# Optimization experiments

Hardware: AMD Instinct MI355X
Metric: run time of the kernel (lower is better)

Reference implementation:

```python
import jax, jax.numpy as jnp
import numpy as np

N_QUBITS = 8
INPUT_DIM = 256
SEQ_LEN = 256
BATCH = 512


def qgate(theta, x):
    # Closed-form expectation of the PennyLane circuit:
    #   RX(x_i) then RY(theta_i) on each wire (from |0>), then CNOT chain 0->1->...->n-1,
    #   measure <Z_k>.  Single-wire <Z_j> = cos(x_j) * cos(theta_j); CNOT chain maps
    #   Z_k -> Z_0 Z_1 ... Z_k in the Heisenberg picture, so on the product state
    #   <Z_k> = prod_{j<=k} cos(x_j) cos(theta_j).
    # x: (B, n_wires), theta: (n_wires,)
    return jnp.cumprod(jnp.cos(x) * jnp.cos(theta), axis=-1)


def setup_inputs() -> dict:
    key = jax.random.key(0)
    ks = jax.random.split(key, 14)
    d_in = INPUT_DIM + N_QUBITS  # concat([x, hx]) -> 264
    lin_scale = 1.0 / np.sqrt(d_in)
    inp = {
        "inputs": jax.random.normal(ks[0], (SEQ_LEN, BATCH, INPUT_DIM), dtype=jnp.float32),
        "Wf": jax.random.normal(ks[1], (N_QUBITS, d_in), dtype=jnp.float32) * lin_scale,
        "bf": jax.random.normal(ks[2], (N_QUBITS,), dtype=jnp.float32) * lin_scale,
        "Wi": jax.random.normal(ks[3], (N_QUBITS, d_in), dtype=jnp.float32) * lin_scale,
        "bi": jax.random.normal(ks[4], (N_QUBITS,), dtype=jnp.float32) * lin_scale,
        "Wu": jax.random.normal(ks[5], (N_QUBITS, d_in), dtype=jnp.float32) * lin_scale,
        "bu": jax.random.normal(ks[6], (N_QUBITS,), dtype=jnp.float32) * lin_scale,
        "Wo": jax.random.normal(ks[7], (N_QUBITS, d_in), dtype=jnp.float32) * lin_scale,
        "bo": jax.random.normal(ks[8], (N_QUBITS,), dtype=jnp.float32) * lin_scale,
        "pf": jax.random.normal(ks[9], (N_QUBITS,), dtype=jnp.float32),
        "pi_": jax.random.normal(ks[10], (N_QUBITS,), dtype=jnp.float32),
        "pu": jax.random.normal(ks[11], (N_QUBITS,), dtype=jnp.float32),
        "po": jax.random.normal(ks[12], (N_QUBITS,), dtype=jnp.float32),
    }
    return inp


def reference(inputs, Wf, bf, Wi, bi, Wu, bu, Wo, bo, pf, pi_, pu, po):
    B = inputs.shape[1]
    H = pf.shape[0]  # hidden_dim == n_qubits

    def step(carry, x):
        hx, cx = carry
        comb = jnp.concatenate([x, hx], axis=1)  # (B, input_dim + H)
        f = jax.nn.sigmoid(qgate(pf, comb @ Wf.T + bf))
        i = jax.nn.sigmoid(qgate(pi_, comb @ Wi.T + bi))
        g = jnp.tanh(qgate(pu, comb @ Wu.T + bu))
        o = jax.nn.sigmoid(qgate(po, comb @ Wo.T + bo))
        cx = f * cx + i * g
        hx = o * jnp.tanh(cx)
        return (hx, cx), hx

    init = (jnp.zeros((B, H), dtype=inputs.dtype), jnp.zeros((B, H), dtype=inputs.dtype))
    (hx, cx), stacked = jax.lax.scan(step, init, inputs)
    return stacked, hx, cx
```

## Files before the change

kernel.cpp:

```cpp
#include <hip/hip_runtime.h>
#include <hip/hip_bf16.h>


#define SEQ   256
#define BATCH 512
#define DIN   256
#define NROWS (SEQ * BATCH)
#define DCOMB 264
#define MCHUNKS 4

typedef __attribute__((ext_vector_type(8))) short short8;
typedef __attribute__((ext_vector_type(4))) float f32x4;
typedef __attribute__((ext_vector_type(2))) float f32x2;

__device__ __forceinline__ short f2bf(float f) {
    union { __hip_bfloat16 h; short s; } u;
    u.h = __float2bfloat16(f);
    return u.s;
}
__device__ __forceinline__ float bf2f(short s) {
    union { short s; __hip_bfloat16 h; } u;
    u.s = s;
    return __bfloat162float(u.h);
}

__device__ __forceinline__ short8 pack8(float4 a, float4 b) {
    union { short8 s8; int i[4]; } u;
    union { __hip_bfloat162 h; int i; } v;
    v.h = __float22bfloat162_rn(make_float2(a.x, a.y)); u.i[0] = v.i;
    v.h = __float22bfloat162_rn(make_float2(a.z, a.w)); u.i[1] = v.i;
    v.h = __float22bfloat162_rn(make_float2(b.x, b.y)); u.i[2] = v.i;
    v.h = __float22bfloat162_rn(make_float2(b.z, b.w)); u.i[3] = v.i;
    return u.s8;
}

__global__ __launch_bounds__(256) void qlstm_gemm(
    const float* __restrict__ X,
    const float* __restrict__ Wf, const float* __restrict__ Wi,
    const float* __restrict__ Wu, const float* __restrict__ Wo,
    const float* __restrict__ bfv, const float* __restrict__ biv,
    const float* __restrict__ buv, const float* __restrict__ bov,
    float* __restrict__ Z)
{
    const int l   = threadIdx.x & 63;
    const int wid = threadIdx.x >> 6;
    const int lm  = l & 15;
    const int lk  = l >> 4;

    const float* Wg[4] = {Wf, Wi, Wu, Wo};
    const float* Bg[4] = {bfv, biv, buv, bov};

    short8 Bhi[2][8], Blo[2][8];
    float bias[2];
    #pragma unroll
    for (int nt = 0; nt < 2; ++nt) {
        const int c = nt * 16 + lm;
        const float* wrow = Wg[c & 3] + (c >> 2) * DCOMB;
        bias[nt] = Bg[c & 3][c >> 2];
        #pragma unroll
        for (int ks = 0; ks < 8; ++ks) {
            const float* p = wrow + ks * 32 + lk * 8;
            const float4 w0 = *(const float4*)p;
            const float4 w1 = *(const float4*)(p + 4);
            const float wv[8] = {w0.x, w0.y, w0.z, w0.w, w1.x, w1.y, w1.z, w1.w};
            #pragma unroll
            for (int j = 0; j < 8; ++j) {
                const short hi = f2bf(wv[j]);
                Bhi[nt][ks][j] = hi;
                Blo[nt][ks][j] = f2bf(wv[j] - bf2f(hi));
            }
        }
    }

    #pragma unroll
    for (int ch = 0; ch < MCHUNKS; ++ch) {
        const int row0 = (blockIdx.x * MCHUNKS + ch) * 64 + wid * 16;
        const float* xbase = X + (long)(row0 + lm) * DIN + lk * 8;

        float4 xv[16];
        #pragma unroll
        for (int i = 0; i < 16; ++i)
            xv[i] = *(const float4*)(xbase + (i >> 1) * 32 + (i & 1) * 4);

        f32x4 acc0 = (f32x4){bias[0], bias[0], bias[0], bias[0]};
        f32x4 acc1 = (f32x4){bias[1], bias[1], bias[1], bias[1]};
        #pragma unroll
        for (int ks = 0; ks < 8; ++ks) {
            const short8 a = pack8(xv[2 * ks], xv[2 * ks + 1]);
            acc0 = __builtin_amdgcn_mfma_f32_16x16x32_bf16(a, Bhi[0][ks], acc0, 0, 0, 0);
            acc0 = __builtin_amdgcn_mfma_f32_16x16x32_bf16(a, Blo[0][ks], acc0, 0, 0, 0);
            acc1 = __builtin_amdgcn_mfma_f32_16x16x32_bf16(a, Bhi[1][ks], acc1, 0, 0, 0);
            acc1 = __builtin_amdgcn_mfma_f32_16x16x32_bf16(a, Blo[1][ks], acc1, 0, 0, 0);
        }

        #pragma unroll
        for (int r = 0; r < 4; ++r) {
            Z[(long)(row0 + lk * 4 + r) * 32 + lm]      = acc0[r];
            Z[(long)(row0 + lk * 4 + r) * 32 + 16 + lm] = acc1[r];
        }
    }
}

#define DPP_ROR(V, S) \
    __int_as_float(__builtin_amdgcn_update_dpp(__float_as_int(V), __float_as_int(V), 0x120 | (S), 0xF, 0xF, false))
#define QP(V, CTRL) \
    __int_as_float(__builtin_amdgcn_update_dpp(__float_as_int(V), __float_as_int(V), (CTRL), 0xF, 0xF, false))

#define PSTG2(A, D) { \
    float s0_ = __int_as_float(__builtin_amdgcn_update_dpp(one_i, __float_as_int(A.x), 0x110 | (D), 0xF, 0xF, false)); \
    float s1_ = __int_as_float(__builtin_amdgcn_update_dpp(one_i, __float_as_int(A.y), 0x110 | (D), 0xF, 0xF, false)); \
    A *= (f32x2){s0_, s1_}; }

#define PF 8

__global__ __launch_bounds__(64, 1) void qlstm_scan(
    const float* __restrict__ Z,
    const float* __restrict__ Wf, const float* __restrict__ Wi,
    const float* __restrict__ Wu, const float* __restrict__ Wo,
    const float* __restrict__ pf, const float* __restrict__ pi_,
    const float* __restrict__ pu, const float* __restrict__ po,
    float* __restrict__ out)
{
    const int tx  = threadIdx.x;
    const int q   = tx & 15;
    const int kq  = q >> 1;
    const int hi  = q & 1;
    const int b   = (blockIdx.x * 64 + tx) >> 4;
    const int oidx = b * 8 + kq;
    const int woff = kq * DCOMB + DIN;

    const float* WgA = hi ? Wu : Wf;
    const float* WgB = hi ? Wo : Wi;
    f32x2 wp[8];
    #pragma unroll
    for (int s = 0; s < 8; ++s) {
        const int j = (kq - s) & 7;
        wp[s] = (f32x2){WgA[woff + j], WgB[woff + j]};
    }
    const f32x2 cth = (f32x2){__cosf((hi ? pu : pf)[kq]),
                              __cosf((hi ? po : pi_)[kq])};

    const float SK1 = 0.25f, SK2 = -0.0208333333f, SK3 = 0.0020833333f,
                SK4 = -0.00021082f;
    const f32x2 k0 = (f32x2){hi ? 0.0f : 0.5f, 0.5f};
    const f32x2 k1 = (f32x2){hi ? 0.9999016f : SK1, SK1};
    const f32x2 k2 = (f32x2){hi ? -0.3310485f : SK2, SK2};
    const f32x2 k3 = (f32x2){hi ? 0.1204423f : SK3, SK3};
    const f32x2 k4 = (f32x2){hi ? -0.0277012f : SK4, SK4};

    const int one_i = __float_as_int(1.0f);

    float hx = 0.0f, cx = 0.0f;
    const float2* __restrict__ Zv2 = (const float2*)Z;
    const int zoff = b * 16 + q;
    float* __restrict__ outp = out + oidx;

    float2 ring[PF];
    #pragma unroll
    for (int i = 0; i < PF; ++i) ring[i] = Zv2[(i << 13) + zoff];

    for (int t0 = 0; t0 < SEQ; t0 += PF) {
        #pragma unroll
        for (int u = 0; u < PF; ++u) {
            const int t = t0 + u;
            const float2 z2 = ring[u];
            int tn = t + PF; if (tn > SEQ - 1) tn = SEQ - 1;
            ring[u] = Zv2[(tn << 13) + zoff];

            const float h0 = hx;
            const float h1 = DPP_ROR(hx, 2),  h2 = DPP_ROR(hx, 4);
            const float h3 = DPP_ROR(hx, 6),  h4 = DPP_ROR(hx, 8);
            const float h5 = DPP_ROR(hx, 10), h6 = DPP_ROR(hx, 12);
            const float h7 = DPP_ROR(hx, 14);

            f32x2 e0 = (f32x2){h0, h0} * wp[0] + (f32x2){h1, h1} * wp[1];
            f32x2 e1 = (f32x2){h2, h2} * wp[2] + (f32x2){h3, h3} * wp[3];
            f32x2 e2 = (f32x2){h4, h4} * wp[4] + (f32x2){h5, h5} * wp[5];
            f32x2 e3 = (f32x2){h6, h6} * wp[6] + (f32x2){h7, h7} * wp[7];
            const f32x2 p = (((f32x2){z2.x, z2.y} + e0) + (e1 + e2)) + e3;

            f32x2 A = (f32x2){__cosf(p.x), __cosf(p.y)} * cth;
            PSTG2(A, 2) PSTG2(A, 4) PSTG2(A, 8)

            const f32x2 t2 = A * A;
            f32x2 r = k3 + t2 * k4;
            r = k2 + t2 * r;
            r = k1 + t2 * r;
            const f32x2 P = k0 + A * r;

            const float f_all = QP(P.x, 0xA0);
            const float u_all = QP(P.x, 0xF5);
            const float i_all = QP(P.y, 0xA0);
            const float o_all = QP(P.y, 0xF5);

            cx = fmaf(f_all, cx, i_all * u_all);

            const float tq  = cx * cx;
            const float num = cx * fmaf(tq, fmaf(tq, 1.0f, 105.0f), 945.0f);
            const float den = fmaf(tq, fmaf(tq, 15.0f, 420.0f), 945.0f);
            const float tc  = num * __builtin_amdgcn_rcpf(den);

            hx = o_all * tc;

            outp[t << 12] = hx;
        }
    }
    if (hi == 0) {
        out[NROWS * 8 + oidx]        = hx;
        out[NROWS * 8 + 4096 + oidx] = cx;
    }
}

extern "C" void kernel_launch(void* const* d_in, const int* in_sizes, int n_in,
                              void* d_out, int out_size, void* d_ws, size_t ws_size,
                              hipStream_t stream) {
    const float* X   = (const float*)d_in[0];
    const float* Wf  = (const float*)d_in[1];
    const float* bfv = (const float*)d_in[2];
    const float* Wi  = (const float*)d_in[3];
    const float* biv = (const float*)d_in[4];
    const float* Wu  = (const float*)d_in[5];
    const float* buv = (const float*)d_in[6];
    const float* Wo  = (const float*)d_in[7];
    const float* bov = (const float*)d_in[8];
    const float* pf  = (const float*)d_in[9];
    const float* pi_ = (const float*)d_in[10];
    const float* pu  = (const float*)d_in[11];
    const float* po  = (const float*)d_in[12];
    float* out = (float*)d_out;
    float* Z   = (float*)d_ws;

    qlstm_gemm<<<NROWS / (64 * MCHUNKS), 256, 0, stream>>>(
        X, Wf, Wi, Wu, Wo, bfv, biv, buv, bov, Z);
    qlstm_scan<<<128, 64, 0, stream>>>(Z, Wf, Wi, Wu, Wo, pf, pi_, pu, po, out);
}
```

Before: 262.5 us.

## Fuse input GEMM and recurrent scan into one kernel staging Z in LDS

Replaces the separate MFMA GEMM kernel and the scan kernel with a single fused kernel. Each 512-thread block handles two batch elements. It first computes their input projections for all timesteps with bf16 hi/lo MFMA, using weight fragments staged in shared memory, and writes them to a padded LDS buffer. One wave then runs the recurrence, reading from LDS instead of global memory. This removes the global round trip of the intermediate Z buffer and one kernel launch. In exchange, the GEMM and the scan are serialized inside each block, the LDS footprint is large, and half of the scan wave's lanes redundantly recompute duplicate batch elements.

```diff
diff --git a/kernel.cpp b/kernel.cpp
--- a/kernel.cpp
+++ b/kernel.cpp
@@ -7,7 +7,7 @@
 #define DIN   256
 #define NROWS (SEQ * BATCH)
 #define DCOMB 264
-#define MCHUNKS 4
+#define ZSTR  34
 
 typedef __attribute__((ext_vector_type(8))) short short8;
 typedef __attribute__((ext_vector_type(4))) float f32x4;
@@ -34,98 +34,102 @@
     return u.s8;
 }
 
-__global__ __launch_bounds__(256) void qlstm_gemm(
+#define DPP_ROR(V, S) \
+    __int_as_float(__builtin_amdgcn_update_dpp(__float_as_int(V), __float_as_int(V), 0x120 | (S), 0xF, 0xF, false))
+#define QP(V, CTRL) \
+    __int_as_float(__builtin_amdgcn_update_dpp(__float_as_int(V), __float_as_int(V), (CTRL), 0xF, 0xF, false))
+#define PSTG2(A, D) { \
+    float s0_ = __int_as_float(__builtin_amdgcn_update_dpp(one_i, __float_as_int(A.x), 0x110 | (D), 0xF, 0xF, false)); \
+    float s1_ = __int_as_float(__builtin_amdgcn_update_dpp(one_i, __float_as_int(A.y), 0x110 | (D), 0xF, 0xF, false)); \
+    A *= (f32x2){s0_, s1_}; }
+
+__global__ __launch_bounds__(512, 2) void qlstm_fused(
     const float* __restrict__ X,
     const float* __restrict__ Wf, const float* __restrict__ Wi,
     const float* __restrict__ Wu, const float* __restrict__ Wo,
     const float* __restrict__ bfv, const float* __restrict__ biv,
     const float* __restrict__ buv, const float* __restrict__ bov,
-    float* __restrict__ Z)
-{
-    const int l   = threadIdx.x & 63;
-    const int wid = threadIdx.x >> 6;
-    const int lm  = l & 15;
-    const int lk  = l >> 4;
-
-    const float* Wg[4] = {Wf, Wi, Wu, Wo};
-    const float* Bg[4] = {bfv, biv, buv, bov};
-
-    short8 Bhi[2][8], Blo[2][8];
-    float bias[2];
-    #pragma unroll
-    for (int nt = 0; nt < 2; ++nt) {
-        const int c = nt * 16 + lm;
-        const float* wrow = Wg[c & 3] + (c >> 2) * DCOMB;
-        bias[nt] = Bg[c & 3][c >> 2];
-        #pragma unroll
-        for (int ks = 0; ks < 8; ++ks) {
-            const float* p = wrow + ks * 32 + lk * 8;
-            const float4 w0 = *(const float4*)p;
-            const float4 w1 = *(const float4*)(p + 4);
-            const float wv[8] = {w0.x, w0.y, w0.z, w0.w, w1.x, w1.y, w1.z, w1.w};
-            #pragma unroll
-            for (int j = 0; j < 8; ++j) {
-                const short hi = f2bf(wv[j]);
-                Bhi[nt][ks][j] = hi;
-                Blo[nt][ks][j] = f2bf(wv[j] - bf2f(hi));
-            }
-        }
-    }
-
-    #pragma unroll
-    for (int ch = 0; ch < MCHUNKS; ++ch) {
-        const int row0 = (blockIdx.x * MCHUNKS + ch) * 64 + wid * 16;
-        const float* xbase = X + (long)(row0 + lm) * DIN + lk * 8;
-
-        float4 xv[16];
-        #pragma unroll
-        for (int i = 0; i < 16; ++i)
-            xv[i] = *(const float4*)(xbase + (i >> 1) * 32 + (i & 1) * 4);
-
-        f32x4 acc0 = (f32x4){bias[0], bias[0], bias[0], bias[0]};
-        f32x4 acc1 = (f32x4){bias[1], bias[1], bias[1], bias[1]};
-        #pragma unroll
-        for (int ks = 0; ks < 8; ++ks) {
-            const short8 a = pack8(xv[2 * ks], xv[2 * ks + 1]);
-            acc0 = __builtin_amdgcn_mfma_f32_16x16x32_bf16(a, Bhi[0][ks], acc0, 0, 0, 0);
-            acc0 = __builtin_amdgcn_mfma_f32_16x16x32_bf16(a, Blo[0][ks], acc0, 0, 0, 0);
-            acc1 = __builtin_amdgcn_mfma_f32_16x16x32_bf16(a, Bhi[1][ks], acc1, 0, 0, 0);
-            acc1 = __builtin_amdgcn_mfma_f32_16x16x32_bf16(a, Blo[1][ks], acc1, 0, 0, 0);
-        }
-
-        #pragma unroll
-        for (int r = 0; r < 4; ++r) {
-            Z[(long)(row0 + lk * 4 + r) * 32 + lm]      = acc0[r];
-            Z[(long)(row0 + lk * 4 + r) * 32 + 16 + lm] = acc1[r];
-        }
-    }
-}
-
-#define DPP_ROR(V, S) \
-    __int_as_float(__builtin_amdgcn_update_dpp(__float_as_int(V), __float_as_int(V), 0x120 | (S), 0xF, 0xF, false))
-#define QP(V, CTRL) \
-    __int_as_float(__builtin_amdgcn_update_dpp(__float_as_int(V), __float_as_int(V), (CTRL), 0xF, 0xF, false))
-
-#define PSTG2(A, D) { \
-    float s0_ = __int_as_float(__builtin_amdgcn_update_dpp(one_i, __float_as_int(A.x), 0x110 | (D), 0xF, 0xF, false)); \
-    float s1_ = __int_as_float(__builtin_amdgcn_update_dpp(one_i, __float_as_int(A.y), 0x110 | (D), 0xF, 0xF, false)); \
-    A *= (f32x2){s0_, s1_}; }
-
-#define PF 8
-
-__global__ __launch_bounds__(64, 1) void qlstm_scan(
-    const float* __restrict__ Z,
-    const float* __restrict__ Wf, const float* __restrict__ Wi,
-    const float* __restrict__ Wu, const float* __restrict__ Wo,
     const float* __restrict__ pf, const float* __restrict__ pi_,
     const float* __restrict__ pu, const float* __restrict__ po,
     float* __restrict__ out)
 {
+    __shared__ short8 Wl[2048];
+    __shared__ float Zl[512 * ZSTR];
+
     const int tx  = threadIdx.x;
+    const int l   = tx & 63;
+    const int wid = tx >> 6;
+    const int lm  = l & 15;
+    const int lk  = l >> 4;
+    const int B0  = blockIdx.x;
+
+    const float* Wg[4] = {Wf, Wi, Wu, Wo};
+    const float* Bg[4] = {bfv, biv, buv, bov};
+
+    #pragma unroll
+    for (int e = 0; e < 4; ++e) {
+        const int ent  = tx + e * 512;
+        const int lane = ent & 63;
+        const int ks   = (ent >> 6) & 7;
+        const int hl   = (ent >> 9) & 1;
+        const int nt   = (ent >> 10) & 1;
+        const int elm  = lane & 15, elk = lane >> 4;
+        const int c    = nt * 16 + elm;
+        const float* wrow = Wg[c & 3] + (c >> 2) * DCOMB + ks * 32 + elk * 8;
+        short8 fr;
+        #pragma unroll
+        for (int j = 0; j < 8; ++j) {
+            const float v = wrow[j];
+            const short h16 = f2bf(v);
+            fr[j] = hl ? f2bf(v - bf2f(h16)) : h16;
+        }
+        Wl[ent] = fr;
+    }
+
+    float bias0, bias1;
+    { const int c0 = lm;      bias0 = Bg[c0 & 3][c0 >> 2];
+      const int c1 = 16 + lm; bias1 = Bg[c1 & 3][c1 >> 2]; }
+
+    __syncthreads();
+
+    #pragma unroll
+    for (int p = 0; p < 4; ++p) {
+        const int r0 = p * 128 + wid * 16;
+        const int r  = r0 + lm;
+        const float* xbase =
+            X + ((long)(r >> 1) * BATCH + B0 * 2 + (r & 1)) * DIN + lk * 8;
+
+        float4 xv[16];
+        #pragma unroll
+        for (int i = 0; i < 16; ++i)
+            xv[i] = *(const float4*)(xbase + (i >> 1) * 32 + (i & 1) * 4);
+
+        f32x4 acc0 = (f32x4){bias0, bias0, bias0, bias0};
+        f32x4 acc1 = (f32x4){bias1, bias1, bias1, bias1};
+        #pragma unroll
+        for (int ks = 0; ks < 8; ++ks) {
+            const short8 a = pack8(xv[2 * ks], xv[2 * ks + 1]);
+            acc0 = __builtin_amdgcn_mfma_f32_16x16x32_bf16(a, Wl[ks * 64 + l],        acc0, 0, 0, 0);
+            acc0 = __builtin_amdgcn_mfma_f32_16x16x32_bf16(a, Wl[(8  + ks) * 64 + l], acc0, 0, 0, 0);
+            acc1 = __builtin_amdgcn_mfma_f32_16x16x32_bf16(a, Wl[(16 + ks) * 64 + l], acc1, 0, 0, 0);
+            acc1 = __builtin_amdgcn_mfma_f32_16x16x32_bf16(a, Wl[(24 + ks) * 64 + l], acc1, 0, 0, 0);
+        }
+
+        #pragma unroll
+        for (int rr = 0; rr < 4; ++rr) {
+            Zl[(r0 + lk * 4 + rr) * ZSTR + lm]      = acc0[rr];
+            Zl[(r0 + lk * 4 + rr) * ZSTR + 16 + lm] = acc1[rr];
+        }
+    }
+    __syncthreads();
+
+    if (tx >= 64) return;
+
     const int q   = tx & 15;
     const int kq  = q >> 1;
     const int hi  = q & 1;
-    const int b   = (blockIdx.x * 64 + tx) >> 4;
+    const int bl  = (tx >> 4) & 1;
+    const int b   = B0 * 2 + bl;
     const int oidx = b * 8 + kq;
     const int woff = kq * DCOMB + DIN;
 
@@ -151,61 +155,57 @@
     const int one_i = __float_as_int(1.0f);
 
     float hx = 0.0f, cx = 0.0f;
-    const float2* __restrict__ Zv2 = (const float2*)Z;
-    const int zoff = b * 16 + q;
+    const int zbase = bl * ZSTR + 2 * q;
     float* __restrict__ outp = out + oidx;
 
-    float2 ring[PF];
-    #pragma unroll
-    for (int i = 0; i < PF; ++i) ring[i] = Zv2[(i << 13) + zoff];
-
-    for (int t0 = 0; t0 < SEQ; t0 += PF) {
-        #pragma unroll
-        for (int u = 0; u < PF; ++u) {
-            const int t = t0 + u;
-            const float2 z2 = ring[u];
-            int tn = t + PF; if (tn > SEQ - 1) tn = SEQ - 1;
-            ring[u] = Zv2[(tn << 13) + zoff];
-
-            const float h0 = hx;
-            const float h1 = DPP_ROR(hx, 2),  h2 = DPP_ROR(hx, 4);
-            const float h3 = DPP_ROR(hx, 6),  h4 = DPP_ROR(hx, 8);
-            const float h5 = DPP_ROR(hx, 10), h6 = DPP_ROR(hx, 12);
-            const float h7 = DPP_ROR(hx, 14);
-
-            f32x2 e0 = (f32x2){h0, h0} * wp[0] + (f32x2){h1, h1} * wp[1];
-            f32x2 e1 = (f32x2){h2, h2} * wp[2] + (f32x2){h3, h3} * wp[3];
-            f32x2 e2 = (f32x2){h4, h4} * wp[4] + (f32x2){h5, h5} * wp[5];
-            f32x2 e3 = (f32x2){h6, h6} * wp[6] + (f32x2){h7, h7} * wp[7];
-            const f32x2 p = (((f32x2){z2.x, z2.y} + e0) + (e1 + e2)) + e3;
-
-            f32x2 A = (f32x2){__cosf(p.x), __cosf(p.y)} * cth;
-            PSTG2(A, 2) PSTG2(A, 4) PSTG2(A, 8)
-
-            const f32x2 t2 = A * A;
-            f32x2 r = k3 + t2 * k4;
-            r = k2 + t2 * r;
-            r = k1 + t2 * r;
-            const f32x2 P = k0 + A * r;
-
-            const float f_all = QP(P.x, 0xA0);
-            const float u_all = QP(P.x, 0xF5);
-            const float i_all = QP(P.y, 0xA0);
-            const float o_all = QP(P.y, 0xF5);
-
-            cx = fmaf(f_all, cx, i_all * u_all);
-
-            const float tq  = cx * cx;
-            const float num = cx * fmaf(tq, fmaf(tq, 1.0f, 105.0f), 945.0f);
-            const float den = fmaf(tq, fmaf(tq, 15.0f, 420.0f), 945.0f);
-            const float tc  = num * __builtin_amdgcn_rcpf(den);
-
-            hx = o_all * tc;
-
-            outp[t << 12] = hx;
-        }
-    }
-    if (hi == 0) {
+    f32x2 ring0 = *(const f32x2*)&Zl[zbase];
+    f32x2 ring1 = *(const f32x2*)&Zl[2 * ZSTR + zbase];
+
+    #pragma unroll 4
+    for (int t = 0; t < SEQ; ++t) {
+        const f32x2 z2 = ring0;
+        ring0 = ring1;
+        int tn = t + 2; if (tn > SEQ - 1) tn = SEQ - 1;
+        ring1 = *(const f32x2*)&Zl[tn * (2 * ZSTR) + zbase];
+
+        const float h0 = hx;
+        const float h1 = DPP_ROR(hx, 2),  h2 = DPP_ROR(hx, 4);
+        const float h3 = DPP_ROR(hx, 6),  h4 = DPP_ROR(hx, 8);
+        const float h5 = DPP_ROR(hx, 10), h6 = DPP_ROR(hx, 12);
+        const float h7 = DPP_ROR(hx, 14);
+
+        f32x2 e0 = (f32x2){h0, h0} * wp[0] + (f32x2){h1, h1} * wp[1];
+        f32x2 e1 = (f32x2){h2, h2} * wp[2] + (f32x2){h3, h3} * wp[3];
+        f32x2 e2 = (f32x2){h4, h4} * wp[4] + (f32x2){h5, h5} * wp[5];
+        f32x2 e3 = (f32x2){h6, h6} * wp[6] + (f32x2){h7, h7} * wp[7];
+        const f32x2 p = ((z2 + e0) + (e1 + e2)) + e3;
+
+        f32x2 A = (f32x2){__cosf(p.x), __cosf(p.y)} * cth;
+        PSTG2(A, 2) PSTG2(A, 4) PSTG2(A, 8)
+
+        const f32x2 t2 = A * A;
+        f32x2 rr = k3 + t2 * k4;
+        rr = k2 + t2 * rr;
+        rr = k1 + t2 * rr;
+        const f32x2 P = k0 + A * rr;
+
+        const float f_all = QP(P.x, 0xA0);
+        const float u_all = QP(P.x, 0xF5);
+        const float i_all = QP(P.y, 0xA0);
+        const float o_all = QP(P.y, 0xF5);
+
+        cx = fmaf(f_all, cx, i_all * u_all);
+
+        const float tq  = cx * cx;
+        const float num = cx * fmaf(tq, fmaf(tq, 1.0f, 105.0f), 945.0f);
+        const float den = fmaf(tq, fmaf(tq, 15.0f, 420.0f), 945.0f);
+        const float tc  = num * __builtin_amdgcn_rcpf(den);
+
+        hx = o_all * tc;
+
+        outp[t << 12] = hx;
+    }
+    if (hi == 0 && tx < 32) {
         out[NROWS * 8 + oidx]        = hx;
         out[NROWS * 8 + 4096 + oidx] = cx;
     }
@@ -228,9 +228,8 @@
     const float* pu  = (const float*)d_in[11];
     const float* po  = (const float*)d_in[12];
     float* out = (float*)d_out;
-    float* Z   = (float*)d_ws;
-
-    qlstm_gemm<<<NROWS / (64 * MCHUNKS), 256, 0, stream>>>(
-        X, Wf, Wi, Wu, Wo, bfv, biv, buv, bov, Z);
-    qlstm_scan<<<128, 64, 0, stream>>>(Z, Wf, Wi, Wu, Wo, pf, pi_, pu, po, out);
-}
+    (void)d_ws; (void)ws_size;
+
+    qlstm_fused<<<512 / 2, 512, 0, stream>>>(
+        X, Wf, Wi, Wu, Wo, bfv, biv, buv, bov, pf, pi_, pu, po, out);
+}
```

Result: faster. 254.2 us (-3.2%).
